# Kernel optimization log

Hardware: AMD Instinct MI355X
Metric: run time of the kernel (lower is better)

Reference implementation:

```python
import math
import jax, jax.numpy as jnp
import numpy as np

EMBED_SIZE = 1024
NUM_HEADS = 16
HEAD_DIM = EMBED_SIZE // NUM_HEADS
N, L = 8, 1024
MASK_FILL = -1e3  # value used by masked_fill in the original (NOT -inf)
SCALE = 1.0 / math.sqrt(EMBED_SIZE)  # original divides by embed_size**0.5, not head_dim


def setup_inputs() -> dict:
    key = jax.random.key(0)
    ks = jax.random.split(key, 7)
    values = jax.random.normal(ks[0], (N, L, EMBED_SIZE), dtype=jnp.float32)
    keys_t = jax.random.normal(ks[1], (N, L, EMBED_SIZE), dtype=jnp.float32)
    queries = jax.random.normal(ks[2], (N, L, EMBED_SIZE), dtype=jnp.float32)
    attn_mask = jax.random.randint(ks[3], (1, 1, L, L), 0, 2, dtype=jnp.int32)
    scr_key_padding_mask = jax.random.randint(ks[4], (N, 1, 1, L), 0, 2, dtype=jnp.int32)
    # fc_out: nn.Linear(embed_size, embed_size) with bias
    fc_w = jax.random.normal(ks[5], (EMBED_SIZE, EMBED_SIZE), dtype=jnp.float32) * (1.0 / math.sqrt(EMBED_SIZE))
    fc_b = jax.random.normal(ks[6], (EMBED_SIZE,), dtype=jnp.float32) * 0.01
    return {"values": values, "keys": keys_t, "queries": queries,
            "fc_w": fc_w, "fc_b": fc_b,
            "attn_mask": attn_mask, "scr_key_padding_mask": scr_key_padding_mask}


def reference(values, keys, queries, fc_w, fc_b, attn_mask, scr_key_padding_mask):
    n, q_len, e = queries.shape
    k_len = keys.shape[1]
    h, d = NUM_HEADS, HEAD_DIM
    # NOTE: the original defines per-head Linear projections but never applies them
    v = values.reshape(n, k_len, h, d)
    k = keys.reshape(n, k_len, h, d)
    q = queries.reshape(n, q_len, h, d)
    energy = jnp.einsum('nqhd,nkhd->nhqk', q, k)  # [n, h, q, k]
    am = attn_mask[:, :, :k_len, :k_len]
    energy = jnp.where(am == 0, MASK_FILL, energy)
    energy = jnp.where(scr_key_padding_mask == 0, MASK_FILL, energy)
    attention = jax.nn.softmax(energy * SCALE, axis=3)
    out = jnp.einsum('nhql,nlhd->nqhd', attention, v).reshape(n, q_len, h * d)
    return out @ fc_w.T + fc_b
```

## Files before the change

kernel.cpp:

```cpp
#include <hip/hip_runtime.h>

#define L_SEQ 1024
#define EMB 1024
#define NH 16
#define HD 64

typedef _Float16 half8 __attribute__((ext_vector_type(8)));
typedef _Float16 half4v __attribute__((ext_vector_type(4)));
typedef __fp16 h2 __attribute__((ext_vector_type(2)));
typedef float f32x4 __attribute__((ext_vector_type(4)));
typedef float f32x16 __attribute__((ext_vector_type(16)));
typedef float fvec4 __attribute__((ext_vector_type(4)));
typedef unsigned int u32;
typedef u32 u32x4 __attribute__((ext_vector_type(4)));
typedef unsigned long long u64;

constexpr float C2 = 0.045084220027780106f;

constexpr int PP = 72;

__device__ __forceinline__ void async16(const void* g, void* l) {
    __builtin_amdgcn_global_load_lds((const __attribute__((address_space(1))) u32*)g,
                                     (__attribute__((address_space(3))) u32*)l, 16, 0, 0);
}

__global__ void pack_mask_kernel(const int* __restrict__ am, u32* __restrict__ bits,
                                 const int* __restrict__ pad, u32* __restrict__ pbits) {
    const int i = blockIdx.x * 256 + threadIdx.x;
    const int lane = threadIdx.x & 63;
    u64 b = __ballot(am[i] != 0);
    if (lane == 0)       bits[i >> 5] = (u32)b;
    else if (lane == 32) bits[i >> 5] = (u32)(b >> 32);
    if (blockIdx.x < 32) {
        const int j = blockIdx.x * 256 + threadIdx.x;
        u64 pb = __ballot(pad[j] != 0);
        if (lane == 0)       pbits[j >> 5] = (u32)pb;
        else if (lane == 32) pbits[j >> 5] = (u32)(pb >> 32);
    }
}

__global__ void convert_w_kernel(const float* __restrict__ w, _Float16* __restrict__ o) {
    size_t i = ((size_t)blockIdx.x * blockDim.x + threadIdx.x) * 4;
    fvec4 v = *(const fvec4*)(w + i);
    half4v h;
#pragma unroll
    for (int j = 0; j < 4; ++j) h[j] = (_Float16)v[j];
    *(half4v*)(o + i) = h;
}

__global__ __launch_bounds__(256) void cvt_kv_kernel(
    const float* __restrict__ keys, const float* __restrict__ values,
    _Float16* __restrict__ K16, _Float16* __restrict__ Vt16)
{
    __shared__ __align__(16) _Float16 Vt[64 * PP];
    const int tid = threadIdx.x;
    const int kt = blockIdx.x, h = blockIdx.y, n = blockIdx.z;
    const int kbase = kt * 64;
    const int r = tid >> 2, c0 = (tid & 3) * 16;
    const int nh = n * NH + h;

    {
        const float* src = keys + ((size_t)(n * L_SEQ + kbase + r)) * EMB + h * HD + c0;
        fvec4 a0 = *(const fvec4*)(src),     a1 = *(const fvec4*)(src + 4);
        fvec4 a2 = *(const fvec4*)(src + 8), a3 = *(const fvec4*)(src + 12);
        half8 o0, o1;
#pragma unroll
        for (int j = 0; j < 4; ++j) {
            o0[j] = (_Float16)(a0[j] * C2); o0[j + 4] = (_Float16)(a1[j] * C2);
            o1[j] = (_Float16)(a2[j] * C2); o1[j + 4] = (_Float16)(a3[j] * C2);
        }
        _Float16* dst = K16 + ((size_t)nh * L_SEQ + kbase + r) * HD + c0;
        *(half8*)dst = o0; *(half8*)(dst + 8) = o1;
    }
    {
        const float* src = values + ((size_t)(n * L_SEQ + kbase + r)) * EMB + h * HD + c0;
        fvec4 vv[4];
        vv[0] = *(const fvec4*)(src);     vv[1] = *(const fvec4*)(src + 4);
        vv[2] = *(const fvec4*)(src + 8); vv[3] = *(const fvec4*)(src + 12);
#pragma unroll
        for (int i = 0; i < 16; ++i)
            Vt[(c0 + i) * PP + r] = (_Float16)vv[i >> 2][i & 3];
    }
    __syncthreads();
    {
        const int d = tid >> 2, k0 = (tid & 3) * 16;
        half8 v0 = *(const half8*)(&Vt[d * PP + k0]);
        half8 v1 = *(const half8*)(&Vt[d * PP + k0 + 8]);
        _Float16* dst = Vt16 + ((size_t)nh * HD + d) * L_SEQ + kbase + k0;
        *(half8*)dst = v0; *(half8*)(dst + 8) = v1;
    }
}

__global__ __launch_bounds__(256, 3) void attn_kernel(
    const _Float16* __restrict__ K16, const _Float16* __restrict__ Vt16,
    const float* __restrict__ queries, const u32* __restrict__ mbits,
    const u32* __restrict__ pbits, _Float16* __restrict__ out_f16)
{
    __shared__ __align__(16) _Float16 K_lds[2][64 * 64];
    __shared__ __align__(16) _Float16 V_lds[2][64 * 64];
    __shared__ __align__(8)  u32 mtab[32];

    const int tid  = threadIdx.x;
    const int lane = tid & 63;
    const int wv   = tid >> 6;
    const int l32  = lane & 31;
    const int hi   = lane >> 5;
    const int bid  = blockIdx.x;
    const int nh = bid & 127, qt = bid >> 7;
    const int n = nh >> 4, h = nh & 15;
    const int qbase = qt * 128;
    const int q = qbase + wv * 32 + l32;
    const int rsw = l32 & 7;

    const _Float16* Kt_base = K16 + (size_t)nh * L_SEQ * HD;
    const _Float16* Vt_base = Vt16 + (size_t)nh * HD * L_SEQ;
    const int gch = (lane & 7) ^ ((lane >> 3) & 7);

    auto stage = [&](int buf, int kt) {
        const int kbase = kt * 64;
#pragma unroll
        for (int s2 = 0; s2 < 2; ++s2) {
            const int row = wv * 16 + s2 * 8 + (lane >> 3);
            async16(Kt_base + (size_t)(kbase + row) * HD + gch * 8,
                    &K_lds[buf][(wv * 16 + s2 * 8) * 64]);
            async16(Vt_base + (size_t)row * L_SEQ + kbase + gch * 8,
                    &V_lds[buf][(wv * 16 + s2 * 8) * 64]);
        }
    };

    uint2 wm_cur = *(const uint2*)(&mbits[(size_t)q * 32]);
    u32 pl_cur = pbits[n << 5];
    u32 ph_cur = pbits[(n << 5) + 1];
    stage(0, 0);

    if (tid < 16) {
        mtab[tid * 2]     = ((tid & 1) ? 0x3C00u : 0u) | ((tid & 2) ? 0x3C000000u : 0u);
        mtab[tid * 2 + 1] = ((tid & 4) ? 0x3C00u : 0u) | ((tid & 8) ? 0x3C000000u : 0u);
    }

    half8 qf[4];
    {
        const float* qp = queries + ((size_t)(n * L_SEQ + q)) * EMB + h * HD;
#pragma unroll
        for (int c = 0; c < 4; ++c) {
            fvec4 a = *(const fvec4*)(qp + c * 16 + hi * 8);
            fvec4 b = *(const fvec4*)(qp + c * 16 + hi * 8 + 4);
#pragma unroll
            for (int j = 0; j < 4; ++j) { qf[c][j] = (_Float16)a[j]; qf[c][j + 4] = (_Float16)b[j]; }
        }
    }

    f32x16 Ov[2];
#pragma unroll
    for (int dt = 0; dt < 2; ++dt)
#pragma unroll
        for (int r = 0; r < 16; ++r) Ov[dt][r] = 0.f;
    float lsum = 0.f;
    const h2 one2 = {(__fp16)1.f, (__fp16)1.f};

    int cur = 0;
#pragma unroll 2
    for (int kt = 0; kt < L_SEQ / 64; ++kt) {
        __syncthreads();

        uint2 wm_next = {0u, 0u};
        u32 pl_next = 0u, ph_next = 0u;
        if (kt + 1 < L_SEQ / 64) {
            wm_next = *(const uint2*)(&mbits[(size_t)q * 32 + (kt + 1) * 2]);
            pl_next = pbits[(n << 5) + ((kt + 1) << 1)];
            ph_next = pbits[(n << 5) + ((kt + 1) << 1) + 1];
            stage(cur ^ 1, kt + 1);
        }

        u32 w[2];
        w[0] = wm_cur.x & pl_cur;
        w[1] = wm_cur.y & ph_cur;

        f32x16 St[2];
#pragma unroll
        for (int i = 0; i < 2; ++i)
#pragma unroll
            for (int r = 0; r < 16; ++r) St[i][r] = 0.f;

        const _Float16* kb = &K_lds[cur][0];
        __builtin_amdgcn_s_setprio(1);
#pragma unroll
        for (int c = 0; c < 4; ++c) {
            const int ch = ((2 * c + hi) ^ rsw) * 8;
            half8 kf0 = *(const half8*)(kb + l32 * 64 + ch);
            half8 kf1 = *(const half8*)(kb + (32 + l32) * 64 + ch);
            St[0] = __builtin_amdgcn_mfma_f32_32x32x16_f16(kf0, qf[c], St[0], 0, 0, 0);
            St[1] = __builtin_amdgcn_mfma_f32_32x32x16_f16(kf1, qf[c], St[1], 0, 0, 0);
        }
        __builtin_amdgcn_s_setprio(0);

        u32 pa[4][4];
#pragma unroll
        for (int i = 0; i < 2; ++i) {
#pragma unroll
            for (int rgp = 0; rgp < 2; ++rgp) {
                const int rg_a = 2 * rgp, rg_b = 2 * rgp + 1;
                const u32 m4a = (w[i] >> (8 * rg_a + 4 * hi)) & 15u;
                const u32 m4b = (w[i] >> (8 * rg_b + 4 * hi)) & 15u;
                const uint2 mma = *(const uint2*)(&mtab[m4a * 2]);
                const uint2 mmb = *(const uint2*)(&mtab[m4b * 2]);
                const float pa0 = __builtin_amdgcn_exp2f(St[i][4 * rg_a + 0]);
                const float pa1 = __builtin_amdgcn_exp2f(St[i][4 * rg_a + 1]);
                const float pa2 = __builtin_amdgcn_exp2f(St[i][4 * rg_a + 2]);
                const float pa3 = __builtin_amdgcn_exp2f(St[i][4 * rg_a + 3]);
                const float pb0 = __builtin_amdgcn_exp2f(St[i][4 * rg_b + 0]);
                const float pb1 = __builtin_amdgcn_exp2f(St[i][4 * rg_b + 1]);
                const float pb2 = __builtin_amdgcn_exp2f(St[i][4 * rg_b + 2]);
                const float pb3 = __builtin_amdgcn_exp2f(St[i][4 * rg_b + 3]);
                const h2 a0 = __builtin_amdgcn_cvt_pkrtz(pa0, pa1) * __builtin_bit_cast(h2, mma.x);
                const h2 a1 = __builtin_amdgcn_cvt_pkrtz(pa2, pa3) * __builtin_bit_cast(h2, mma.y);
                const h2 b0 = __builtin_amdgcn_cvt_pkrtz(pb0, pb1) * __builtin_bit_cast(h2, mmb.x);
                const h2 b1 = __builtin_amdgcn_cvt_pkrtz(pb2, pb3) * __builtin_bit_cast(h2, mmb.y);
                lsum = __builtin_amdgcn_fdot2(a0, one2, lsum, false);
                lsum = __builtin_amdgcn_fdot2(a1, one2, lsum, false);
                lsum = __builtin_amdgcn_fdot2(b0, one2, lsum, false);
                lsum = __builtin_amdgcn_fdot2(b1, one2, lsum, false);
                u32 A0 = __builtin_bit_cast(u32, a0), A1 = __builtin_bit_cast(u32, a1);
                u32 B0 = __builtin_bit_cast(u32, b0), B1 = __builtin_bit_cast(u32, b1);
                asm("v_permlane32_swap_b32 %0, %1" : "+v"(A0), "+v"(B0));
                asm("v_permlane32_swap_b32 %0, %1" : "+v"(A1), "+v"(B1));
                const int ks = i * 2 + rgp;
                pa[ks][0] = A0; pa[ks][1] = A1; pa[ks][2] = B0; pa[ks][3] = B1;
            }
        }

        const _Float16* vb = &V_lds[cur][0];
        __builtin_amdgcn_s_setprio(1);
#pragma unroll
        for (int ks = 0; ks < 4; ++ks) {
            u32x4 pw = {pa[ks][0], pa[ks][1], pa[ks][2], pa[ks][3]};
            half8 pB = __builtin_bit_cast(half8, pw);
            const int ch = ((2 * ks + hi) ^ rsw) * 8;
            half8 vf0 = *(const half8*)(vb + l32 * 64 + ch);
            half8 vf1 = *(const half8*)(vb + (32 + l32) * 64 + ch);
            Ov[0] = __builtin_amdgcn_mfma_f32_32x32x16_f16(pB, vf0, Ov[0], 0, 0, 0);
            Ov[1] = __builtin_amdgcn_mfma_f32_32x32x16_f16(pB, vf1, Ov[1], 0, 0, 0);
        }
        __builtin_amdgcn_s_setprio(0);

        wm_cur = wm_next; pl_cur = pl_next; ph_cur = ph_next;
        cur ^= 1;
    }

    lsum += __shfl_xor(lsum, 32);
    float linv[16];
#pragma unroll
    for (int reg = 0; reg < 16; ++reg) {
        const int qrel = (reg & 3) + 8 * (reg >> 2) + 4 * hi;
        linv[reg] = 1.0f / fmaxf(__shfl(lsum, qrel), 1e-25f);
    }
#pragma unroll
    for (int reg = 0; reg < 16; ++reg) {
        const int qrow = qbase + wv * 32 + (reg & 3) + 8 * (reg >> 2) + 4 * hi;
        _Float16* op = out_f16 + ((size_t)(n * L_SEQ + qrow)) * EMB + h * HD;
        op[l32]      = (_Float16)(Ov[0][reg] * linv[reg]);
        op[32 + l32] = (_Float16)(Ov[1][reg] * linv[reg]);
    }
}

__global__ __launch_bounds__(256) void fc_kernel(
    const _Float16* __restrict__ A, const _Float16* __restrict__ W,
    const float* __restrict__ bias, float* __restrict__ C)
{
    __shared__ __align__(16) _Float16 As[2][128 * 64];
    __shared__ __align__(16) _Float16 Ws[2][128 * 64];

    const int tid = threadIdx.x;
    const int lane = tid & 63;
    const int wv = tid >> 6;
    const int l16 = lane & 15;
    const int quad = lane >> 4;
    const int wm = (wv >> 1) * 64, wn = (wv & 1) * 64;
    const int Mb = blockIdx.x * 128, Nb = blockIdx.y * 128;
    const int xr = l16 & 7;

    auto stage = [&](int buf, int k0) {
#pragma unroll
        for (int s = 0; s < 4; ++s) {
            const int row = wv * 32 + s * 8 + (lane >> 3);
            const int sc = (lane & 7) ^ (row & 7);
            async16(A + (size_t)(Mb + row) * EMB + k0 + sc * 8, &As[buf][(wv * 32 + s * 8) * 64]);
            async16(W + (size_t)(Nb + row) * EMB + k0 + sc * 8, &Ws[buf][(wv * 32 + s * 8) * 64]);
        }
    };

    f32x4 acc[4][4];
#pragma unroll
    for (int i = 0; i < 4; ++i)
#pragma unroll
        for (int j = 0; j < 4; ++j) acc[i][j] = (f32x4){0.f, 0.f, 0.f, 0.f};

    stage(0, 0);
    int cur = 0;
#pragma unroll 2
    for (int k0 = 0; k0 < EMB; k0 += 64) {
        __syncthreads();
        if (k0 + 64 < EMB) stage(cur ^ 1, k0 + 64);

        half8 af[4][2], bf[4][2];
#pragma unroll
        for (int i = 0; i < 4; ++i)
#pragma unroll
            for (int kk = 0; kk < 2; ++kk) {
                const int ch = (((kk * 4 + quad) ^ xr)) * 8;
                af[i][kk] = *(const half8*)(&As[cur][(wm + i * 16 + l16) * 64 + ch]);
                bf[i][kk] = *(const half8*)(&Ws[cur][(wn + i * 16 + l16) * 64 + ch]);
            }
        __builtin_amdgcn_s_setprio(1);
#pragma unroll
        for (int i = 0; i < 4; ++i)
#pragma unroll
            for (int j = 0; j < 4; ++j)
#pragma unroll
                for (int kk = 0; kk < 2; ++kk)
                    acc[i][j] = __builtin_amdgcn_mfma_f32_16x16x32_f16(af[i][kk], bf[j][kk], acc[i][j], 0, 0, 0);
        __builtin_amdgcn_s_setprio(0);
        cur ^= 1;
    }

#pragma unroll
    for (int i = 0; i < 4; ++i) {
        const int m = Mb + wm + i * 16 + quad * 4;
#pragma unroll
        for (int j = 0; j < 4; ++j) {
            const int jc = Nb + wn + j * 16 + l16;
            const float b = bias[jc];
#pragma unroll
            for (int reg = 0; reg < 4; ++reg)
                C[(size_t)(m + reg) * EMB + jc] = acc[i][j][reg] + b;
        }
    }
}

extern "C" void kernel_launch(void* const* d_in, const int* in_sizes, int n_in,
                              void* d_out, int out_size, void* d_ws, size_t ws_size,
                              hipStream_t stream) {
    const float* values  = (const float*)d_in[0];
    const float* keys    = (const float*)d_in[1];
    const float* queries = (const float*)d_in[2];
    const float* fc_w    = (const float*)d_in[3];
    const float* fc_b    = (const float*)d_in[4];
    const int*   amask   = (const int*)d_in[5];
    const int*   pmask   = (const int*)d_in[6];
    float* out = (float*)d_out;

    char* w = (char*)d_ws;
    _Float16* attn_out = (_Float16*)w;
    _Float16* w_f16    = (_Float16*)(w + (size_t)16 * 1024 * 1024);
    u32*      mbits    = (u32*)(w + (size_t)18 * 1024 * 1024);
    u32*      pbits    = (u32*)(w + (size_t)18 * 1024 * 1024 + 128 * 1024);
    _Float16* K16      = (_Float16*)(w + (size_t)19 * 1024 * 1024);
    _Float16* Vt16     = (_Float16*)(w + (size_t)35 * 1024 * 1024);

    pack_mask_kernel<<<4096, 256, 0, stream>>>(amask, mbits, pmask, pbits);
    convert_w_kernel<<<1024, 256, 0, stream>>>(fc_w, w_f16);
    cvt_kv_kernel<<<dim3(16, 16, 8), 256, 0, stream>>>(keys, values, K16, Vt16);
    attn_kernel<<<1024, 256, 0, stream>>>(K16, Vt16, queries, mbits, pbits, attn_out);
    fc_kernel<<<dim3(64, 8), 256, 0, stream>>>(attn_out, w_f16, fc_b, out);
}
```

Baseline: 224.8 us.

## Merge prep kernels, repad V transpose buffer, raise attention occupancy hint

Combines the mask-packing and weight-conversion kernels into one launch to save a kernel launch. Changes the LDS row pitch of the V transpose scratch from 72 to 66 halves to reduce bank conflicts on the scattered writes, reading rows back as 32-bit words because the new pitch breaks 16-byte alignment. Raises the attention kernel's launch_bounds min-blocks from 3 to 4, which may force register spilling.

```diff
diff --git a/kernel.cpp b/kernel.cpp
--- a/kernel.cpp
+++ b/kernel.cpp
@@ -17,35 +17,35 @@
 
 constexpr float C2 = 0.045084220027780106f;
 
-constexpr int PP = 72;
+constexpr int PP = 66;
 
 __device__ __forceinline__ void async16(const void* g, void* l) {
     __builtin_amdgcn_global_load_lds((const __attribute__((address_space(1))) u32*)g,
                                      (__attribute__((address_space(3))) u32*)l, 16, 0, 0);
 }
 
-__global__ void pack_mask_kernel(const int* __restrict__ am, u32* __restrict__ bits,
-                                 const int* __restrict__ pad, u32* __restrict__ pbits) {
-    const int i = blockIdx.x * 256 + threadIdx.x;
+__global__ void prep_kernel(const int* __restrict__ am, u32* __restrict__ bits,
+                            const int* __restrict__ pad, u32* __restrict__ pbits,
+                            const float* __restrict__ w, _Float16* __restrict__ o) {
+    const int b = blockIdx.x;
+    const int i = b * 256 + threadIdx.x;
     const int lane = threadIdx.x & 63;
-    u64 b = __ballot(am[i] != 0);
-    if (lane == 0)       bits[i >> 5] = (u32)b;
-    else if (lane == 32) bits[i >> 5] = (u32)(b >> 32);
-    if (blockIdx.x < 32) {
-        const int j = blockIdx.x * 256 + threadIdx.x;
-        u64 pb = __ballot(pad[j] != 0);
-        if (lane == 0)       pbits[j >> 5] = (u32)pb;
-        else if (lane == 32) pbits[j >> 5] = (u32)(pb >> 32);
-    }
-}
-
-__global__ void convert_w_kernel(const float* __restrict__ w, _Float16* __restrict__ o) {
-    size_t i = ((size_t)blockIdx.x * blockDim.x + threadIdx.x) * 4;
-    fvec4 v = *(const fvec4*)(w + i);
-    half4v h;
-#pragma unroll
-    for (int j = 0; j < 4; ++j) h[j] = (_Float16)v[j];
-    *(half4v*)(o + i) = h;
+    u64 bal = __ballot(am[i] != 0);
+    if (lane == 0)       bits[i >> 5] = (u32)bal;
+    else if (lane == 32) bits[i >> 5] = (u32)(bal >> 32);
+    if (b < 32) {
+        u64 pb = __ballot(pad[i] != 0);
+        if (lane == 0)       pbits[i >> 5] = (u32)pb;
+        else if (lane == 32) pbits[i >> 5] = (u32)(pb >> 32);
+    }
+    if (b < 1024) {
+        size_t j = (size_t)i * 4;
+        fvec4 v = *(const fvec4*)(w + j);
+        half4v hh;
+#pragma unroll
+        for (int k = 0; k < 4; ++k) hh[k] = (_Float16)v[k];
+        *(half4v*)(o + j) = hh;
+    }
 }
 
 __global__ __launch_bounds__(256) void cvt_kv_kernel(
@@ -84,14 +84,19 @@
     __syncthreads();
     {
         const int d = tid >> 2, k0 = (tid & 3) * 16;
-        half8 v0 = *(const half8*)(&Vt[d * PP + k0]);
-        half8 v1 = *(const half8*)(&Vt[d * PP + k0 + 8]);
+        const u32* vr = (const u32*)((const char*)Vt + (size_t)d * (PP * 2) + 2 * k0);
+        u32 a[8];
+#pragma unroll
+        for (int m = 0; m < 8; ++m) a[m] = vr[m];
+        u32x4 lo = {a[0], a[1], a[2], a[3]};
+        u32x4 hi2 = {a[4], a[5], a[6], a[7]};
         _Float16* dst = Vt16 + ((size_t)nh * HD + d) * L_SEQ + kbase + k0;
-        *(half8*)dst = v0; *(half8*)(dst + 8) = v1;
-    }
-}
-
-__global__ __launch_bounds__(256, 3) void attn_kernel(
+        *(half8*)dst = __builtin_bit_cast(half8, lo);
+        *(half8*)(dst + 8) = __builtin_bit_cast(half8, hi2);
+    }
+}
+
+__global__ __launch_bounds__(256, 4) void attn_kernel(
     const _Float16* __restrict__ K16, const _Float16* __restrict__ Vt16,
     const float* __restrict__ queries, const u32* __restrict__ mbits,
     const u32* __restrict__ pbits, _Float16* __restrict__ out_f16)
@@ -357,8 +362,7 @@
     _Float16* K16      = (_Float16*)(w + (size_t)19 * 1024 * 1024);
     _Float16* Vt16     = (_Float16*)(w + (size_t)35 * 1024 * 1024);
 
-    pack_mask_kernel<<<4096, 256, 0, stream>>>(amask, mbits, pmask, pbits);
-    convert_w_kernel<<<1024, 256, 0, stream>>>(fc_w, w_f16);
+    prep_kernel<<<4096, 256, 0, stream>>>(amask, mbits, pmask, pbits, fc_w, w_f16);
     cvt_kv_kernel<<<dim3(16, 16, 8), 256, 0, stream>>>(keys, values, K16, Vt16);
     attn_kernel<<<1024, 256, 0, stream>>>(K16, Vt16, queries, mbits, pbits, attn_out);
     fc_kernel<<<dim3(64, 8), 256, 0, stream>>>(attn_out, w_f16, fc_b, out);
```

Measured after the change: 231.8 us. 3.1% more time.
